# Optimization experiments

Hardware: AMD Instinct MI355X
Metric: run time of the kernel (lower is better)

Reference implementation:

```python
import jax, jax.numpy as jnp
import numpy as np

N = 50000        # nodes
E = 800000       # edges (avg degree 16)
F = 64           # in/out feature dim (scatter into zeros_like(x) forces out==in)
H = 128          # hidden dim
CIN = 2 * F + 1  # combined_features dim


def setup_inputs() -> dict:
    key = jax.random.key(0)
    ks = jax.random.split(key, 12)
    x = jax.random.normal(ks[0], (N, F), dtype=jnp.float32)
    pos = jax.random.normal(ks[1], (N, 3), dtype=jnp.float32)
    edge_index = jax.random.randint(ks[2], (2, E), 0, N, dtype=jnp.int64)
    s1 = 1.0 / np.sqrt(CIN)
    s2 = 1.0 / np.sqrt(H)
    W1x = jax.random.uniform(ks[3], (CIN, H), jnp.float32, -s1, s1)
    b1x = jax.random.uniform(ks[4], (H,), jnp.float32, -s1, s1)
    W2x = jax.random.uniform(ks[5], (H, F), jnp.float32, -s2, s2)
    b2x = jax.random.uniform(ks[6], (F,), jnp.float32, -s2, s2)
    W1p = jax.random.uniform(ks[7], (CIN, H), jnp.float32, -s1, s1)
    b1p = jax.random.uniform(ks[8], (H,), jnp.float32, -s1, s1)
    W2p = jax.random.uniform(ks[9], (H, 1), jnp.float32, -s2, s2)
    b2p = jax.random.uniform(ks[10], (1,), jnp.float32, -s2, s2)
    return {"x": x, "pos": pos, "edge_index": edge_index,
            "W1x": W1x, "b1x": b1x, "W2x": W2x, "b2x": b2x,
            "W1p": W1p, "b1p": b1p, "W2p": W2p, "b2p": b2p}


def reference(x, pos, edge_index, W1x, b1x, W2x, b2x, W1p, b1p, W2p, b2p):
    row, col = edge_index[0], edge_index[1]
    rel_pos = pos[row] - pos[col]                              # [E, 3]
    dist_sq = jnp.sum(rel_pos * rel_pos, axis=-1, keepdims=True)  # [E, 1]
    combined = jnp.concatenate([x[row], x[col], dist_sq], axis=-1)  # [E, 2F+1]
    # phi_x: Linear -> SiLU -> Linear
    msg_x = jax.nn.silu(combined @ W1x + b1x) @ W2x + b2x      # [E, F]
    aggregated_x = jax.ops.segment_sum(msg_x, col, num_segments=x.shape[0])
    # phi_pos: Linear -> SiLU -> Linear (scalar weight per edge)
    weight_pos = jax.nn.silu(combined @ W1p + b1p) @ W2p + b2p  # [E, 1]
    pos_update = weight_pos * rel_pos                           # [E, 3]
    aggregated_pos = jax.ops.segment_sum(pos_update, col, num_segments=pos.shape[0])
    return aggregated_x, aggregated_pos
```

## Files before the change

kernel.cpp:

```cpp
#include <hip/hip_runtime.h>

typedef short short8 __attribute__((ext_vector_type(8)));
typedef float floatx4 __attribute__((ext_vector_type(4)));

__device__ __forceinline__ unsigned short f2bf(float f) {
  unsigned int u = __float_as_uint(f);
  u += 0x7FFFu + ((u >> 16) & 1u);
  return (unsigned short)(u >> 16);
}

#if __has_builtin(__builtin_amdgcn_cvt_pk_bf16_f32)
typedef __bf16 bf16x2_t __attribute__((ext_vector_type(2)));
__device__ __forceinline__ unsigned int pk2bf(float lo, float hi) {
  bf16x2_t v = __builtin_amdgcn_cvt_pk_bf16_f32(lo, hi);
  return __builtin_bit_cast(unsigned int, v);
}
#else
__device__ __forceinline__ unsigned int pk2bf(float lo, float hi) {
  return (unsigned)f2bf(lo) | ((unsigned)f2bf(hi) << 16);
}
#endif

__global__ __launch_bounds__(256) void k_setup(
    float* __restrict__ out, int out_n,
    int* __restrict__ hist, int N,
    const float* __restrict__ x, unsigned short* __restrict__ xb, int nx,
    const float* __restrict__ W1x, const float* __restrict__ W1p,
    const float* __restrict__ b1x, const float* __restrict__ b1p,
    const float* __restrict__ W2x, unsigned short* __restrict__ wbuf,
    int b1, int b2, int b3)
{
  int blk = blockIdx.x, t = threadIdx.x;
  if (blk < b1) {
    int i = (blk * 256 + t) * 4;
    if (i + 4 <= out_n) {
      *(float4*)(out + i) = make_float4(0.f, 0.f, 0.f, 0.f);
    } else {
      for (int k = i; k < out_n; ++k) out[k] = 0.f;
    }
  } else if (blk < b2) {
    int i = (blk - b1) * 256 + t;
    if (i < N) hist[i] = 0;
  } else if (blk < b3) {
    int i = ((blk - b2) * 256 + t) * 8;
    if (i < nx) {
      float4 a = *(const float4*)(x + i);
      float4 b = *(const float4*)(x + i + 4);
      uint4 o;
      o.x = pk2bf(a.x, a.y); o.y = pk2bf(a.z, a.w);
      o.z = pk2bf(b.x, b.y); o.w = pk2bf(b.z, b.w);
      *(uint4*)(xb + i) = o;
    }
  } else {
    int i = (blk - b3) * 256 + t;
    if (i >= 49152) return;
    float v;
    if (i < 40960) {
      const float* W = (i < 20480) ? W1x : W1p;
      const float* B = (i < 20480) ? b1x : b1p;
      int j = (i < 20480) ? i : i - 20480;
      int jj   = j & 7;
      int lane = (j >> 3) & 63;
      int ks   = (j >> 9) % 5;
      int nt   = j / 2560;
      int k = ks*32 + (lane >> 4)*8 + jj;
      int n = nt*16 + (lane & 15);
      v = (k < 129) ? W[k*128 + n] : (k == 129 ? B[n] : 0.0f);
    } else {
      int j = i - 40960;
      int jj   = j & 7;
      int lane = (j >> 3) & 63;
      int ks   = (j >> 9) & 3;
      int nt   = j >> 11;
      int k = ks*32 + (lane >> 4)*8 + jj;
      int n = nt*16 + (lane & 15);
      v = W2x[k*64 + n];
    }
    wbuf[i] = f2bf(v);
  }
}

__global__ void k_hist(const int* __restrict__ col, int E, int* __restrict__ hist) {
  int i = blockIdx.x * 256 + threadIdx.x;
  if (i < E) atomicAdd(&hist[col[i]], 1);
}

__global__ __launch_bounds__(256) void k_scan_a(const int* __restrict__ hist, int N,
                                                int* __restrict__ excl, int* __restrict__ bsum) {
  __shared__ int wtot[4], wexc[4];
  int t = threadIdx.x, lane = t & 63, w = t >> 6;
  int base = blockIdx.x * 1024 + t * 4;
  int v0 = (base + 0 < N) ? hist[base + 0] : 0;
  int v1 = (base + 1 < N) ? hist[base + 1] : 0;
  int v2 = (base + 2 < N) ? hist[base + 2] : 0;
  int v3 = (base + 3 < N) ? hist[base + 3] : 0;
  int T = v0 + v1 + v2 + v3;
  int inc = T;
  #pragma unroll
  for (int s = 1; s < 64; s <<= 1) {
    int u = __shfl_up(inc, s, 64);
    if (lane >= s) inc += u;
  }
  if (lane == 63) wtot[w] = inc;
  __syncthreads();
  if (t == 0) {
    int a = 0;
    #pragma unroll
    for (int i = 0; i < 4; ++i) { wexc[i] = a; a += wtot[i]; }
    bsum[blockIdx.x] = a;
  }
  __syncthreads();
  int tex = wexc[w] + (inc - T);
  if (base + 0 < N) excl[base + 0] = tex;
  if (base + 1 < N) excl[base + 1] = tex + v0;
  if (base + 2 < N) excl[base + 2] = tex + v0 + v1;
  if (base + 3 < N) excl[base + 3] = tex + v0 + v1 + v2;
}

__global__ __launch_bounds__(256) void k_scatter(
    const int* __restrict__ row, const int* __restrict__ col, int E,
    int* __restrict__ excl, const int* __restrict__ bsum, int NB,
    int2* __restrict__ sedge) {
  __shared__ int boff_sh[64];
  int t = threadIdx.x;
  if (t < 64) {
    int v = (t < NB) ? bsum[t] : 0;
    int inc = v;
    #pragma unroll
    for (int s = 1; s < 64; s <<= 1) {
      int u = __shfl_up(inc, s, 64);
      if (t >= s) inc += u;
    }
    boff_sh[t] = inc - v;
  }
  __syncthreads();
  int i = blockIdx.x * 256 + t;
  if (i < E) {
    int c = col[i];
    int p = atomicAdd(&excl[c], 1) + boff_sh[c >> 10];
    sedge[p] = make_int2(row[i], c);
  }
}

__global__ __launch_bounds__(256) void mp_main(
    const float* __restrict__ x, const unsigned short* __restrict__ xb, int use_xb,
    const float* __restrict__ pos,
    const int2* __restrict__ sedge,
    const int* __restrict__ rowp, const int* __restrict__ colp,
    int E, int sorted, int chunk,
    const float* __restrict__ b2x, const float* __restrict__ W2p,
    const float* __restrict__ b2p,
    const unsigned short* __restrict__ wbuf,
    float* __restrict__ out_x, float* __restrict__ out_pos)
{
  __shared__ __align__(16) unsigned short C_lds[64][168];
  __shared__ float rel_lds[64][3];
  __shared__ int   col_sh[64];
  __shared__ float wsum[4][64];

  const int nblk = (E + 63) >> 6;
  const int logical = (blockIdx.x & 7) * chunk + (blockIdx.x >> 3);
  if (logical >= nblk) return;
  const int e0 = logical * 64;

  const int t    = threadIdx.x;
  const int wv   = t >> 6;
  const int lane = t & 63;
  const int quad = lane >> 4;
  const int lc   = lane & 15;

  const short8* __restrict__ w1x_f = (const short8*)(wbuf);
  const short8* __restrict__ w1p_f = (const short8*)(wbuf + 20480);
  const short8* __restrict__ w2x_f = (const short8*)(wbuf + 40960);

  short8 a1x[2][5], a1p[2][5], a2w[4];
  #pragma unroll
  for (int i = 0; i < 2; ++i) {
    int hti = wv + 4*i;
    #pragma unroll
    for (int ks = 0; ks < 5; ++ks) {
      a1x[i][ks] = w1x_f[(hti*5 + ks)*64 + lane];
      a1p[i][ks] = w1p_f[(hti*5 + ks)*64 + lane];
    }
  }
  #pragma unroll
  for (int ks = 0; ks < 4; ++ks) a2w[ks] = w2x_f[(wv*4 + ks)*64 + lane];

  float wp2[2][4], b2xr[4];
  #pragma unroll
  for (int i = 0; i < 2; ++i)
    #pragma unroll
    for (int r = 0; r < 4; ++r) wp2[i][r] = W2p[(wv + 4*i)*16 + quad*4 + r];
  #pragma unroll
  for (int r = 0; r < 4; ++r) b2xr[r] = b2x[wv*16 + quad*4 + r];
  const float b2ps = b2p[0];

  if (t < 64) {
    int e = e0 + t;
    float rp0 = 0.f, rp1 = 0.f, rp2 = 0.f, dsq = 0.f; int c = -1;
    if (e < E) {
      int r;
      if (sorted) { int2 rc = sedge[e]; r = rc.x; c = rc.y; }
      else        { r = rowp[e]; c = colp[e]; }
      float pr0 = pos[r*3+0], pr1 = pos[r*3+1], pr2 = pos[r*3+2];
      float pc0 = pos[c*3+0], pc1 = pos[c*3+1], pc2 = pos[c*3+2];
      rp0 = pr0 - pc0; rp1 = pr1 - pc1; rp2 = pr2 - pc2;
      dsq = rp0*rp0 + rp1*rp1 + rp2*rp2;
    }
    rel_lds[t][0] = rp0; rel_lds[t][1] = rp1; rel_lds[t][2] = rp2;
    col_sh[t] = c;
    C_lds[t][128] = f2bf(dsq);
    C_lds[t][129] = 0x3F80;
    #pragma unroll
    for (int k = 130; k < 160; ++k) C_lds[t][k] = 0;
  }
  {
    const int s = t >> 2, p = t & 3;
    const int e = e0 + s;
    uint4 r0, r1, c0, c1;
    if (e < E) {
      int r, c;
      if (sorted) { int2 rc = sedge[e]; r = rc.x; c = rc.y; }
      else        { r = rowp[e]; c = colp[e]; }
      if (use_xb) {
        const uint4* xr = (const uint4*)(xb + (size_t)r*64 + p*16);
        const uint4* xc = (const uint4*)(xb + (size_t)c*64 + p*16);
        r0 = xr[0]; r1 = xr[1];
        c0 = xc[0]; c1 = xc[1];
      } else {
        const float4* xr = (const float4*)(x + (size_t)r*64 + p*16);
        const float4* xc = (const float4*)(x + (size_t)c*64 + p*16);
        float4 a0 = xr[0], a1 = xr[1], a2 = xr[2], a3 = xr[3];
        float4 d0 = xc[0], d1 = xc[1], d2 = xc[2], d3 = xc[3];
        r0 = make_uint4(pk2bf(a0.x,a0.y), pk2bf(a0.z,a0.w), pk2bf(a1.x,a1.y), pk2bf(a1.z,a1.w));
        r1 = make_uint4(pk2bf(a2.x,a2.y), pk2bf(a2.z,a2.w), pk2bf(a3.x,a3.y), pk2bf(a3.z,a3.w));
        c0 = make_uint4(pk2bf(d0.x,d0.y), pk2bf(d0.z,d0.w), pk2bf(d1.x,d1.y), pk2bf(d1.z,d1.w));
        c1 = make_uint4(pk2bf(d2.x,d2.y), pk2bf(d2.z,d2.w), pk2bf(d3.x,d3.y), pk2bf(d3.z,d3.w));
      }
    } else {
      r0 = r1 = c0 = c1 = make_uint4(0u, 0u, 0u, 0u);
    }
    uint4* dr = (uint4*)&C_lds[s][p*16];
    dr[0] = r0; dr[1] = r1;
    uint4* dc = (uint4*)&C_lds[s][64 + p*16];
    dc[0] = c0; dc[1] = c1;
  }
  __syncthreads();

  #pragma unroll 1
  for (int et = 0; et < 4; ++et) {
    floatx4 ax0 = {0,0,0,0}, ax1 = {0,0,0,0}, ap0 = {0,0,0,0}, ap1 = {0,0,0,0};
    #pragma unroll
    for (int ks = 0; ks < 5; ++ks) {
      short8 b = *(const short8*)&C_lds[et*16 + lc][ks*32 + quad*8];
      ax0 = __builtin_amdgcn_mfma_f32_16x16x32_bf16(a1x[0][ks], b, ax0, 0, 0, 0);
      ax1 = __builtin_amdgcn_mfma_f32_16x16x32_bf16(a1x[1][ks], b, ax1, 0, 0, 0);
      ap0 = __builtin_amdgcn_mfma_f32_16x16x32_bf16(a1p[0][ks], b, ap0, 0, 0, 0);
      ap1 = __builtin_amdgcn_mfma_f32_16x16x32_bf16(a1p[1][ks], b, ap1, 0, 0, 0);
    }
    float ps = 0.f;
    uint2 hw[2];
    #pragma unroll
    for (int i = 0; i < 2; ++i) {
      floatx4 axx = i ? ax1 : ax0;
      floatx4 app = i ? ap1 : ap0;
      float sx[4];
      #pragma unroll
      for (int r = 0; r < 4; ++r) {
        float h  = axx[r];
        sx[r] = h * __builtin_amdgcn_rcpf(1.f + __expf(-h));
        float hp = app[r];
        float sp = hp * __builtin_amdgcn_rcpf(1.f + __expf(-hp));
        ps += sp * wp2[i][r];
      }
      hw[i] = make_uint2(pk2bf(sx[0], sx[1]), pk2bf(sx[2], sx[3]));
    }
    __syncthreads();
    #pragma unroll
    for (int i = 0; i < 2; ++i)
      *(uint2*)&C_lds[et*16 + lc][(wv + 4*i)*16 + quad*4] = hw[i];
    ps += __shfl_xor(ps, 16, 64);
    ps += __shfl_xor(ps, 32, 64);
    if (lane < 16) wsum[wv][et*16 + lane] = ps;
  }
  __syncthreads();

  #pragma unroll 2
  for (int et = 0; et < 4; ++et) {
    floatx4 acc = {0,0,0,0};
    #pragma unroll
    for (int ks = 0; ks < 4; ++ks) {
      short8 b = *(const short8*)&C_lds[et*16 + lc][ks*32 + quad*8];
      acc = __builtin_amdgcn_mfma_f32_16x16x32_bf16(a2w[ks], b, acc, 0, 0, 0);
    }
    int edge = et*16 + lc;
    int myc = col_sh[edge];
    float v0 = acc[0] + b2xr[0], v1 = acc[1] + b2xr[1];
    float v2 = acc[2] + b2xr[2], v3 = acc[3] + b2xr[3];
    if (sorted) {
      #pragma unroll
      for (int s = 1; s < 16; s <<= 1) {
        int   nc  = __shfl_down(myc, s, 64);
        float n0  = __shfl_down(v0,  s, 64);
        float n1  = __shfl_down(v1,  s, 64);
        float n2  = __shfl_down(v2,  s, 64);
        float n3  = __shfl_down(v3,  s, 64);
        if ((lc + s < 16) && (nc == myc)) { v0 += n0; v1 += n1; v2 += n2; v3 += n3; }
      }
    }
    bool head = (myc >= 0) && (!sorted || lc == 0 || col_sh[edge-1] != myc);
    if (head) {
      float* dst = out_x + (size_t)myc*64 + wv*16 + quad*4;
      atomicAdd(dst + 0, v0);
      atomicAdd(dst + 1, v1);
      atomicAdd(dst + 2, v2);
      atomicAdd(dst + 3, v3);
    }
  }

  if (t < 64) {
    int c = col_sh[t];
    float w = wsum[0][t] + wsum[1][t] + wsum[2][t] + wsum[3][t] + b2ps;
    float p0 = w * rel_lds[t][0], p1 = w * rel_lds[t][1], p2 = w * rel_lds[t][2];
    if (sorted) {
      #pragma unroll
      for (int s = 1; s < 64; s <<= 1) {
        int   nc = __shfl_down(c,  s, 64);
        float n0 = __shfl_down(p0, s, 64);
        float n1 = __shfl_down(p1, s, 64);
        float n2 = __shfl_down(p2, s, 64);
        if ((t + s < 64) && (nc == c)) { p0 += n0; p1 += n1; p2 += n2; }
      }
    }
    bool head = (c >= 0) && (!sorted || t == 0 || col_sh[t-1] != c);
    if (head) {
      atomicAdd(&out_pos[(size_t)c*3 + 0], p0);
      atomicAdd(&out_pos[(size_t)c*3 + 1], p1);
      atomicAdd(&out_pos[(size_t)c*3 + 2], p2);
    }
  }
}

extern "C" void kernel_launch(void* const* d_in, const int* in_sizes, int n_in,
                              void* d_out, int out_size, void* d_ws, size_t ws_size,
                              hipStream_t stream) {
  const float* x   = (const float*)d_in[0];
  const float* pos = (const float*)d_in[1];
  const int*   ei  = (const int*)d_in[2];
  const float* W1x = (const float*)d_in[3];
  const float* b1x = (const float*)d_in[4];
  const float* W2x = (const float*)d_in[5];
  const float* b2x = (const float*)d_in[6];
  const float* W1p = (const float*)d_in[7];
  const float* b1p = (const float*)d_in[8];
  const float* W2p = (const float*)d_in[9];
  const float* b2p = (const float*)d_in[10];

  const int E = in_sizes[2] / 2;
  const int N = in_sizes[0] / 64;
  const int* rowp = ei;
  const int* colp = ei + E;
  float* out_x   = (float*)d_out;
  float* out_pos = out_x + (size_t)N * 64;

  char* ws = (char*)d_ws;
  const size_t xb_bytes = (size_t)N * 64 * 2;
  size_t base = 0;
  int use_xb = 0;
  {
    size_t needA = xb_bytes + 98304 + 200192 + 512 + (size_t)E * 8;
    if (ws_size >= needA) { use_xb = 1; base = xb_bytes; }
  }
  unsigned short* xb   = (unsigned short*)ws;
  unsigned short* wbuf = (unsigned short*)(ws + base);
  int*  off   = (int*)(ws + base + 98304);
  int*  bsum  = (int*)(ws + base + 98304 + 200192);
  int2* sedge = (int2*)(ws + base + 98304 + 200192 + 512);
  const size_t need_sort = base + 98304 + 200192 + 512 + (size_t)E * 8;
  const int use_sort = (ws_size >= need_sort) ? 1 : 0;

  const int nx = N * 64;
  const int nb_out  = (out_size + 1023) / 1024;
  const int nb_hist = use_sort ? (N + 255) / 256 : 0;
  const int nb_xcvt = use_xb ? (nx + 2047) / 2048 : 0;
  const int nb_prep = 192;
  const int b1 = nb_out, b2 = b1 + nb_hist, b3 = b2 + nb_xcvt;
  const int setup_blocks = b3 + nb_prep;
  k_setup<<<setup_blocks, 256, 0, stream>>>(
      (float*)d_out, out_size, off, N, x, xb, nx,
      W1x, W1p, b1x, b1p, W2x, wbuf, b1, b2, b3);

  if (use_sort) {
    const int NB = (N + 1023) / 1024;
    k_hist<<<(E + 255) / 256, 256, 0, stream>>>(colp, E, off);
    k_scan_a<<<NB, 256, 0, stream>>>(off, N, off, bsum);
    k_scatter<<<(E + 255) / 256, 256, 0, stream>>>(rowp, colp, E, off, bsum, NB, sedge);
  }

  const int nblk  = (E + 63) / 64;
  const int chunk = (nblk + 7) / 8;
  mp_main<<<chunk * 8, 256, 0, stream>>>(x, xb, use_xb, pos, sedge, rowp, colp,
                                         E, use_sort, chunk, b2x, W2p, b2p,
                                         wbuf, out_x, out_pos);
}
```

Baseline: 363.5 us.

## Fold dist_sq and bias out of MFMA K dim, use 512-thread blocks

The K dimension of the first layer drops from 160 to 128. The dist_sq column and the bias are now applied as a scalar FMA in fp32 after the MFMA, which removes one MFMA K-step per tile. Blocks grow to 8 waves, each wave owning one 16-wide hidden tile. A separate H_lds buffer means the hidden activations no longer overwrite the input tile, so a barrier inside the loop is dropped. The XCD-chunked block remapping is also removed. The trade is more LDS per block and fewer weight registers per wave, which could change occupancy and L2 locality.

```diff
diff --git a/kernel.cpp b/kernel.cpp
--- a/kernel.cpp
+++ b/kernel.cpp
@@ -26,7 +26,6 @@
     int* __restrict__ hist, int N,
     const float* __restrict__ x, unsigned short* __restrict__ xb, int nx,
     const float* __restrict__ W1x, const float* __restrict__ W1p,
-    const float* __restrict__ b1x, const float* __restrict__ b1p,
     const float* __restrict__ W2x, unsigned short* __restrict__ wbuf,
     int b1, int b2, int b3)
 {
@@ -53,28 +52,17 @@
     }
   } else {
     int i = (blk - b3) * 256 + t;
-    if (i >= 49152) return;
+    if (i >= 40960) return;
+    int jj = i & 7, lane = (i >> 3) & 63, ks = (i >> 9) & 3;
+    int k = ks*32 + (lane >> 4)*8 + jj;
     float v;
-    if (i < 40960) {
-      const float* W = (i < 20480) ? W1x : W1p;
-      const float* B = (i < 20480) ? b1x : b1p;
-      int j = (i < 20480) ? i : i - 20480;
-      int jj   = j & 7;
-      int lane = (j >> 3) & 63;
-      int ks   = (j >> 9) % 5;
-      int nt   = j / 2560;
-      int k = ks*32 + (lane >> 4)*8 + jj;
-      int n = nt*16 + (lane & 15);
-      v = (k < 129) ? W[k*128 + n] : (k == 129 ? B[n] : 0.0f);
+    if (i < 32768) {
+      const float* W = (i < 16384) ? W1x : W1p;
+      int nt = (i >> 11) & 7;
+      v = W[k*128 + nt*16 + (lane & 15)];
     } else {
-      int j = i - 40960;
-      int jj   = j & 7;
-      int lane = (j >> 3) & 63;
-      int ks   = (j >> 9) & 3;
-      int nt   = j >> 11;
-      int k = ks*32 + (lane >> 4)*8 + jj;
-      int n = nt*16 + (lane & 15);
-      v = W2x[k*64 + n];
+      int nt = (i >> 11) & 3;
+      v = W2x[k*64 + nt*16 + (lane & 15)];
     }
     wbuf[i] = f2bf(v);
   }
@@ -142,58 +130,32 @@
   }
 }
 
-__global__ __launch_bounds__(256) void mp_main(
+__global__ __launch_bounds__(512) void mp_main(
     const float* __restrict__ x, const unsigned short* __restrict__ xb, int use_xb,
     const float* __restrict__ pos,
     const int2* __restrict__ sedge,
     const int* __restrict__ rowp, const int* __restrict__ colp,
-    int E, int sorted, int chunk,
+    int E, int sorted,
+    const float* __restrict__ W1x, const float* __restrict__ b1x,
+    const float* __restrict__ W1p, const float* __restrict__ b1p,
     const float* __restrict__ b2x, const float* __restrict__ W2p,
     const float* __restrict__ b2p,
     const unsigned short* __restrict__ wbuf,
     float* __restrict__ out_x, float* __restrict__ out_pos)
 {
-  __shared__ __align__(16) unsigned short C_lds[64][168];
+  __shared__ __align__(16) unsigned short C_lds[64][136];
+  __shared__ __align__(16) unsigned short H_lds[64][136];
+  __shared__ float dsq_sh[64];
   __shared__ float rel_lds[64][3];
   __shared__ int   col_sh[64];
-  __shared__ float wsum[4][64];
-
-  const int nblk = (E + 63) >> 6;
-  const int logical = (blockIdx.x & 7) * chunk + (blockIdx.x >> 3);
-  if (logical >= nblk) return;
-  const int e0 = logical * 64;
+  __shared__ float wsum[8][64];
 
   const int t    = threadIdx.x;
+  const int e0   = blockIdx.x * 64;
   const int wv   = t >> 6;
   const int lane = t & 63;
   const int quad = lane >> 4;
   const int lc   = lane & 15;
-
-  const short8* __restrict__ w1x_f = (const short8*)(wbuf);
-  const short8* __restrict__ w1p_f = (const short8*)(wbuf + 20480);
-  const short8* __restrict__ w2x_f = (const short8*)(wbuf + 40960);
-
-  short8 a1x[2][5], a1p[2][5], a2w[4];
-  #pragma unroll
-  for (int i = 0; i < 2; ++i) {
-    int hti = wv + 4*i;
-    #pragma unroll
-    for (int ks = 0; ks < 5; ++ks) {
-      a1x[i][ks] = w1x_f[(hti*5 + ks)*64 + lane];
-      a1p[i][ks] = w1p_f[(hti*5 + ks)*64 + lane];
-    }
-  }
-  #pragma unroll
-  for (int ks = 0; ks < 4; ++ks) a2w[ks] = w2x_f[(wv*4 + ks)*64 + lane];
-
-  float wp2[2][4], b2xr[4];
-  #pragma unroll
-  for (int i = 0; i < 2; ++i)
-    #pragma unroll
-    for (int r = 0; r < 4; ++r) wp2[i][r] = W2p[(wv + 4*i)*16 + quad*4 + r];
-  #pragma unroll
-  for (int r = 0; r < 4; ++r) b2xr[r] = b2x[wv*16 + quad*4 + r];
-  const float b2ps = b2p[0];
 
   if (t < 64) {
     int e = e0 + t;
@@ -209,88 +171,97 @@
     }
     rel_lds[t][0] = rp0; rel_lds[t][1] = rp1; rel_lds[t][2] = rp2;
     col_sh[t] = c;
-    C_lds[t][128] = f2bf(dsq);
-    C_lds[t][129] = 0x3F80;
-    #pragma unroll
-    for (int k = 130; k < 160; ++k) C_lds[t][k] = 0;
+    dsq_sh[t] = dsq;
   }
   {
-    const int s = t >> 2, p = t & 3;
+    const int s = t >> 3, p = t & 7;
     const int e = e0 + s;
-    uint4 r0, r1, c0, c1;
+    uint4 rv, cv;
     if (e < E) {
       int r, c;
       if (sorted) { int2 rc = sedge[e]; r = rc.x; c = rc.y; }
       else        { r = rowp[e]; c = colp[e]; }
       if (use_xb) {
-        const uint4* xr = (const uint4*)(xb + (size_t)r*64 + p*16);
-        const uint4* xc = (const uint4*)(xb + (size_t)c*64 + p*16);
-        r0 = xr[0]; r1 = xr[1];
-        c0 = xc[0]; c1 = xc[1];
+        rv = *(const uint4*)(xb + (size_t)r*64 + p*8);
+        cv = *(const uint4*)(xb + (size_t)c*64 + p*8);
       } else {
-        const float4* xr = (const float4*)(x + (size_t)r*64 + p*16);
-        const float4* xc = (const float4*)(x + (size_t)c*64 + p*16);
-        float4 a0 = xr[0], a1 = xr[1], a2 = xr[2], a3 = xr[3];
-        float4 d0 = xc[0], d1 = xc[1], d2 = xc[2], d3 = xc[3];
-        r0 = make_uint4(pk2bf(a0.x,a0.y), pk2bf(a0.z,a0.w), pk2bf(a1.x,a1.y), pk2bf(a1.z,a1.w));
-        r1 = make_uint4(pk2bf(a2.x,a2.y), pk2bf(a2.z,a2.w), pk2bf(a3.x,a3.y), pk2bf(a3.z,a3.w));
-        c0 = make_uint4(pk2bf(d0.x,d0.y), pk2bf(d0.z,d0.w), pk2bf(d1.x,d1.y), pk2bf(d1.z,d1.w));
-        c1 = make_uint4(pk2bf(d2.x,d2.y), pk2bf(d2.z,d2.w), pk2bf(d3.x,d3.y), pk2bf(d3.z,d3.w));
+        const float4* xr = (const float4*)(x + (size_t)r*64 + p*8);
+        const float4* xc = (const float4*)(x + (size_t)c*64 + p*8);
+        float4 a0 = xr[0], a1 = xr[1];
+        float4 d0 = xc[0], d1 = xc[1];
+        rv = make_uint4(pk2bf(a0.x,a0.y), pk2bf(a0.z,a0.w), pk2bf(a1.x,a1.y), pk2bf(a1.z,a1.w));
+        cv = make_uint4(pk2bf(d0.x,d0.y), pk2bf(d0.z,d0.w), pk2bf(d1.x,d1.y), pk2bf(d1.z,d1.w));
       }
     } else {
-      r0 = r1 = c0 = c1 = make_uint4(0u, 0u, 0u, 0u);
-    }
-    uint4* dr = (uint4*)&C_lds[s][p*16];
-    dr[0] = r0; dr[1] = r1;
-    uint4* dc = (uint4*)&C_lds[s][64 + p*16];
-    dc[0] = c0; dc[1] = c1;
-  }
+      rv = cv = make_uint4(0u, 0u, 0u, 0u);
+    }
+    *(uint4*)&C_lds[s][p*8]      = rv;
+    *(uint4*)&C_lds[s][64 + p*8] = cv;
+  }
+
+  const short8* __restrict__ w1x_f = (const short8*)(wbuf);
+  const short8* __restrict__ w1p_f = (const short8*)(wbuf + 16384);
+  const short8* __restrict__ w2x_f = (const short8*)(wbuf + 32768);
+
+  const int ht = wv;
+  const int ft = wv & 3;
+  short8 a1x[4], a1p[4], a2w[4];
+  #pragma unroll
+  for (int ks = 0; ks < 4; ++ks) {
+    a1x[ks] = w1x_f[(ht*4 + ks)*64 + lane];
+    a1p[ks] = w1p_f[(ht*4 + ks)*64 + lane];
+    a2w[ks] = w2x_f[(ft*4 + ks)*64 + lane];
+  }
+  const int hidx = ht*16 + quad*4;
+  const int fidx = ft*16 + quad*4;
+  float w128x[4], b1xv[4], w128p[4], b1pv[4], wp2v[4], b2xr[4];
+  #pragma unroll
+  for (int r = 0; r < 4; ++r) {
+    w128x[r] = W1x[16384 + hidx + r];
+    b1xv[r]  = b1x[hidx + r];
+    w128p[r] = W1p[16384 + hidx + r];
+    b1pv[r]  = b1p[hidx + r];
+    wp2v[r]  = W2p[hidx + r];
+    b2xr[r]  = b2x[fidx + r];
+  }
+  const float b2ps = b2p[0];
   __syncthreads();
 
   #pragma unroll 1
   for (int et = 0; et < 4; ++et) {
-    floatx4 ax0 = {0,0,0,0}, ax1 = {0,0,0,0}, ap0 = {0,0,0,0}, ap1 = {0,0,0,0};
-    #pragma unroll
-    for (int ks = 0; ks < 5; ++ks) {
+    floatx4 ax = {0,0,0,0}, ap = {0,0,0,0};
+    #pragma unroll
+    for (int ks = 0; ks < 4; ++ks) {
       short8 b = *(const short8*)&C_lds[et*16 + lc][ks*32 + quad*8];
-      ax0 = __builtin_amdgcn_mfma_f32_16x16x32_bf16(a1x[0][ks], b, ax0, 0, 0, 0);
-      ax1 = __builtin_amdgcn_mfma_f32_16x16x32_bf16(a1x[1][ks], b, ax1, 0, 0, 0);
-      ap0 = __builtin_amdgcn_mfma_f32_16x16x32_bf16(a1p[0][ks], b, ap0, 0, 0, 0);
-      ap1 = __builtin_amdgcn_mfma_f32_16x16x32_bf16(a1p[1][ks], b, ap1, 0, 0, 0);
-    }
-    float ps = 0.f;
-    uint2 hw[2];
-    #pragma unroll
-    for (int i = 0; i < 2; ++i) {
-      floatx4 axx = i ? ax1 : ax0;
-      floatx4 app = i ? ap1 : ap0;
-      float sx[4];
-      #pragma unroll
-      for (int r = 0; r < 4; ++r) {
-        float h  = axx[r];
-        sx[r] = h * __builtin_amdgcn_rcpf(1.f + __expf(-h));
-        float hp = app[r];
-        float sp = hp * __builtin_amdgcn_rcpf(1.f + __expf(-hp));
-        ps += sp * wp2[i][r];
-      }
-      hw[i] = make_uint2(pk2bf(sx[0], sx[1]), pk2bf(sx[2], sx[3]));
-    }
-    __syncthreads();
-    #pragma unroll
-    for (int i = 0; i < 2; ++i)
-      *(uint2*)&C_lds[et*16 + lc][(wv + 4*i)*16 + quad*4] = hw[i];
+      ax = __builtin_amdgcn_mfma_f32_16x16x32_bf16(a1x[ks], b, ax, 0, 0, 0);
+      ap = __builtin_amdgcn_mfma_f32_16x16x32_bf16(a1p[ks], b, ap, 0, 0, 0);
+    }
+    const float dsqv = dsq_sh[et*16 + lc];
+    float ps = 0.f, sx[4];
+    #pragma unroll
+    for (int r = 0; r < 4; ++r) {
+      float hx = ax[r] + dsqv*w128x[r] + b1xv[r];
+      sx[r] = hx * __builtin_amdgcn_rcpf(1.f + __expf(-hx));
+      float hp = ap[r] + dsqv*w128p[r] + b1pv[r];
+      float sp = hp * __builtin_amdgcn_rcpf(1.f + __expf(-hp));
+      ps += sp * wp2v[r];
+    }
+    *(uint2*)&H_lds[et*16 + lc][ht*16 + quad*4] =
+        make_uint2(pk2bf(sx[0], sx[1]), pk2bf(sx[2], sx[3]));
     ps += __shfl_xor(ps, 16, 64);
     ps += __shfl_xor(ps, 32, 64);
     if (lane < 16) wsum[wv][et*16 + lane] = ps;
   }
   __syncthreads();
 
-  #pragma unroll 2
-  for (int et = 0; et < 4; ++et) {
+  const int etb = (wv >> 2) * 2;
+  #pragma unroll
+  for (int eti = 0; eti < 2; ++eti) {
+    const int et = etb + eti;
     floatx4 acc = {0,0,0,0};
     #pragma unroll
     for (int ks = 0; ks < 4; ++ks) {
-      short8 b = *(const short8*)&C_lds[et*16 + lc][ks*32 + quad*8];
+      short8 b = *(const short8*)&H_lds[et*16 + lc][ks*32 + quad*8];
       acc = __builtin_amdgcn_mfma_f32_16x16x32_bf16(a2w[ks], b, acc, 0, 0, 0);
     }
     int edge = et*16 + lc;
@@ -310,7 +281,7 @@
     }
     bool head = (myc >= 0) && (!sorted || lc == 0 || col_sh[edge-1] != myc);
     if (head) {
-      float* dst = out_x + (size_t)myc*64 + wv*16 + quad*4;
+      float* dst = out_x + (size_t)myc*64 + ft*16 + quad*4;
       atomicAdd(dst + 0, v0);
       atomicAdd(dst + 1, v1);
       atomicAdd(dst + 2, v2);
@@ -320,7 +291,8 @@
 
   if (t < 64) {
     int c = col_sh[t];
-    float w = wsum[0][t] + wsum[1][t] + wsum[2][t] + wsum[3][t] + b2ps;
+    float w = wsum[0][t] + wsum[1][t] + wsum[2][t] + wsum[3][t]
+            + wsum[4][t] + wsum[5][t] + wsum[6][t] + wsum[7][t] + b2ps;
     float p0 = w * rel_lds[t][0], p1 = w * rel_lds[t][1], p2 = w * rel_lds[t][2];
     if (sorted) {
       #pragma unroll
@@ -368,27 +340,27 @@
   size_t base = 0;
   int use_xb = 0;
   {
-    size_t needA = xb_bytes + 98304 + 200192 + 512 + (size_t)E * 8;
+    size_t needA = xb_bytes + 81920 + 200192 + 512 + (size_t)E * 8;
     if (ws_size >= needA) { use_xb = 1; base = xb_bytes; }
   }
   unsigned short* xb   = (unsigned short*)ws;
   unsigned short* wbuf = (unsigned short*)(ws + base);
-  int*  off   = (int*)(ws + base + 98304);
-  int*  bsum  = (int*)(ws + base + 98304 + 200192);
-  int2* sedge = (int2*)(ws + base + 98304 + 200192 + 512);
-  const size_t need_sort = base + 98304 + 200192 + 512 + (size_t)E * 8;
+  int*  off   = (int*)(ws + base + 81920);
+  int*  bsum  = (int*)(ws + base + 81920 + 200192);
+  int2* sedge = (int2*)(ws + base + 81920 + 200192 + 512);
+  const size_t need_sort = base + 81920 + 200192 + 512 + (size_t)E * 8;
   const int use_sort = (ws_size >= need_sort) ? 1 : 0;
 
   const int nx = N * 64;
   const int nb_out  = (out_size + 1023) / 1024;
   const int nb_hist = use_sort ? (N + 255) / 256 : 0;
   const int nb_xcvt = use_xb ? (nx + 2047) / 2048 : 0;
-  const int nb_prep = 192;
+  const int nb_prep = 160;
   const int b1 = nb_out, b2 = b1 + nb_hist, b3 = b2 + nb_xcvt;
   const int setup_blocks = b3 + nb_prep;
   k_setup<<<setup_blocks, 256, 0, stream>>>(
       (float*)d_out, out_size, off, N, x, xb, nx,
-      W1x, W1p, b1x, b1p, W2x, wbuf, b1, b2, b3);
+      W1x, W1p, W2x, wbuf, b1, b2, b3);
 
   if (use_sort) {
     const int NB = (N + 1023) / 1024;
@@ -397,9 +369,8 @@
     k_scatter<<<(E + 255) / 256, 256, 0, stream>>>(rowp, colp, E, off, bsum, NB, sedge);
   }
 
-  const int nblk  = (E + 63) / 64;
-  const int chunk = (nblk + 7) / 8;
-  mp_main<<<chunk * 8, 256, 0, stream>>>(x, xb, use_xb, pos, sedge, rowp, colp,
-                                         E, use_sort, chunk, b2x, W2p, b2p,
-                                         wbuf, out_x, out_pos);
-}
+  mp_main<<<(E + 63) / 64, 512, 0, stream>>>(x, xb, use_xb, pos, sedge, rowp, colp,
+                                             E, use_sort,
+                                             W1x, b1x, W1p, b1p, b2x, W2p, b2p,
+                                             wbuf, out_x, out_pos);
+}
```

New measurement: 359.8 us. No clear change (-1.0%).
